# Kernel tuning notes

Measured on AMD Instinct MI355X. Metric: run time of the kernel, lower is better.

## Reference

```python
import jax, jax.numpy as jnp
import numpy as np

N_NODES = 100000
N_EDGES = 3200000
DIM = 64


def setup_inputs() -> dict:
    key = jax.random.key(0)
    k1, k2, k3, k4, k5, k6 = jax.random.split(key, 6)
    lap_rows = jax.random.randint(k1, (N_EDGES,), 0, N_NODES, dtype=jnp.int32)
    lap_cols = jax.random.randint(k2, (N_EDGES,), 0, N_NODES, dtype=jnp.int32)
    # normalized-Laplacian-like positive values
    lap_vals = jax.random.uniform(k3, (N_EDGES,), dtype=jnp.float32) * 0.1
    features = jax.random.normal(k4, (N_NODES, DIM), dtype=jnp.float32)
    scale = 1.0 / np.sqrt(DIM)
    W1 = jax.random.normal(k5, (DIM, DIM), dtype=jnp.float32) * scale
    b1 = jnp.zeros((DIM,), dtype=jnp.float32)
    W2 = jax.random.normal(k6, (DIM, DIM), dtype=jnp.float32) * scale
    b2 = jnp.zeros((DIM,), dtype=jnp.float32)
    return {
        "lap_rows": lap_rows, "lap_cols": lap_cols, "lap_vals": lap_vals,
        "features": features, "W1": W1, "b1": b1, "W2": W2, "b2": b2,
    }


def reference(lap_rows, lap_cols, lap_vals, features, W1, b1, W2, b2):
    # x = L @ features  (COO SpMM: gather source rows, scale, scatter-add to dest)
    msgs = lap_vals[:, None] * features[lap_cols]            # [E, D]
    x = jax.ops.segment_sum(msgs, lap_rows, num_segments=N_NODES)  # [N, D]
    # output = (L+I) E W1 + (L E * E) W2
    inter_part1 = (features + x) @ W1 + b1                   # [N, D_out]
    inter_part2 = (x * features) @ W2 + b2                   # [N, D_out]
    return inter_part1 + inter_part2
```

## Files before the change

kernel.cpp:

```cpp
#include <hip/hip_runtime.h>
#include <hip/hip_fp16.h>

#define DIM 64
#define RPB 64
#define RPB_SHIFT 6
#define SUP_SHIFT 11
#define SB_MAX 64
#define CAP 3072
#define CAPK (CAP / 1024)
#define HTILE_H 16384
#define HTILE1 8192
#define HTILE2 4096

typedef _Float16 half8 __attribute__((ext_vector_type(8)));
typedef float    f32x4 __attribute__((ext_vector_type(4)));
typedef float    f32x2 __attribute__((ext_vector_type(2)));

template <bool HI>
__device__ __forceinline__ __half2 q2h(unsigned int w)
{
    f32x2 f = __builtin_amdgcn_cvt_pk_f32_fp8(w, HI);
    return __floats2half2_rn(f[0], f[1]);
}

__global__ __launch_bounds__(256) void scatter_kernel(
    const int* __restrict__ rows, const int* __restrict__ cols,
    const float* __restrict__ vals, const float* __restrict__ feat,
    float* __restrict__ x, int E)
{
    unsigned long long t = (unsigned long long)blockIdx.x * blockDim.x + threadIdx.x;
    int e = (int)(t >> 6);
    int d = (int)(t & 63);
    if (e >= E) return;
    int r = rows[e];
    int c = cols[e];
    float v = vals[e];
    float f = feat[(size_t)c * DIM + d];
    atomicAdd(&x[(size_t)r * DIM + d], v * f);
}

__global__ __launch_bounds__(256) void cvt_kernel(
    const float* __restrict__ f, __half* __restrict__ h, int n2)
{
    int i = blockIdx.x * blockDim.x + threadIdx.x;
    if (i < n2) {
        float2 v = ((const float2*)f)[i];
        __half2 o;
        o.x = __float2half(v.x);
        o.y = __float2half(v.y);
        ((__half2*)h)[i] = o;
    }
}

__global__ __launch_bounds__(1024) void prep_kernel(
    const float* __restrict__ feat, __half* __restrict__ featH,
    unsigned char* __restrict__ featQ,
    const int* __restrict__ rows, int* __restrict__ gcnt,
    int n8, int NC, int E, int B)
{
    if ((int)blockIdx.x < NC) {
        int i = blockIdx.x * 1024 + threadIdx.x;
        if (i < n8) {
            const float4* src = (const float4*)(feat + (size_t)i * 8);
            float4 a = src[0], b = src[1];
            __half2 h0 = __floats2half2_rn(a.x, a.y);
            __half2 h1 = __floats2half2_rn(a.z, a.w);
            __half2 h2 = __floats2half2_rn(b.x, b.y);
            __half2 h3 = __floats2half2_rn(b.z, b.w);
            float4 ho;
            ho.x = __builtin_bit_cast(float, h0);
            ho.y = __builtin_bit_cast(float, h1);
            ho.z = __builtin_bit_cast(float, h2);
            ho.w = __builtin_bit_cast(float, h3);
            *(float4*)(featH + (size_t)i * 8) = ho;
            unsigned int q0 = __builtin_amdgcn_cvt_pk_fp8_f32(a.x, a.y, 0, false);
            q0 = __builtin_amdgcn_cvt_pk_fp8_f32(a.z, a.w, (int)q0, true);
            unsigned int q1 = __builtin_amdgcn_cvt_pk_fp8_f32(b.x, b.y, 0, false);
            q1 = __builtin_amdgcn_cvt_pk_fp8_f32(b.z, b.w, (int)q1, true);
            uint2 qo; qo.x = q0; qo.y = q1;
            *(uint2*)(featQ + (size_t)i * 8) = qo;
        }
    } else {
        extern __shared__ int lcnt[];
        for (int i = threadIdx.x; i < B; i += 1024) lcnt[i] = 0;
        __syncthreads();
        int base = ((int)blockIdx.x - NC) * HTILE_H;
#pragma unroll
        for (int k = 0; k < HTILE_H / 1024; ++k) {
            int e = base + k * 1024 + threadIdx.x;
            if (e < E) atomicAdd(&lcnt[rows[e] >> RPB_SHIFT], 1);
        }
        __syncthreads();
        for (int i = threadIdx.x; i < B; i += 1024)
            if (lcnt[i]) atomicAdd(&gcnt[i], lcnt[i]);
    }
}

__global__ __launch_bounds__(1024) void scan_kernel(
    const int* __restrict__ gcnt, int* __restrict__ offs, int* __restrict__ cursors,
    int* __restrict__ soffs, int* __restrict__ scursors, int B, int SB, int E)
{
    __shared__ int lds[2048];
    int t = threadIdx.x;
    int c0 = (t < B) ? gcnt[t] : 0;
    int c1 = (t + 1024 < B) ? gcnt[t + 1024] : 0;
    lds[t] = c0;
    lds[t + 1024] = c1;
    __syncthreads();
    for (int off = 1; off < 2048; off <<= 1) {
        int a = (t >= off) ? lds[t - off] : 0;
        int b = lds[t + 1024 - off];
        __syncthreads();
        lds[t] += a;
        lds[t + 1024] += b;
        __syncthreads();
    }
    if (t < B) {
        int e = lds[t] - c0;
        offs[t] = e; cursors[t] = e;
        if ((t & 31) == 0) { soffs[t >> 5] = e; scursors[t >> 5] = e; }
    }
    int t2 = t + 1024;
    if (t2 < B) {
        int e = lds[t2] - c1;
        offs[t2] = e; cursors[t2] = e;
        if ((t2 & 31) == 0) { soffs[t2 >> 5] = e; scursors[t2 >> 5] = e; }
    }
    if (t == 0) { offs[B] = E; soffs[SB] = E; }
}

__global__ __launch_bounds__(1024) void superbin_kernel(
    const int* __restrict__ rows, const int* __restrict__ cols,
    const float* __restrict__ vals, int* __restrict__ scursors,
    unsigned long long* __restrict__ sorted1, int E, int SB)
{
    __shared__ int cnt[SB_MAX];
    __shared__ int bse[SB_MAX];
    const int tid = threadIdx.x;
    if (tid < SB) cnt[tid] = 0;
    __syncthreads();
    const int tbase = blockIdx.x * HTILE1;
    int rr[HTILE1 / 1024];
#pragma unroll
    for (int k = 0; k < HTILE1 / 1024; ++k) {
        int e = tbase + k * 1024 + tid;
        rr[k] = (e < E) ? rows[e] : -1;
        if (rr[k] >= 0) atomicAdd(&cnt[rr[k] >> SUP_SHIFT], 1);
    }
    __syncthreads();
    if (tid < SB) {
        int c = cnt[tid];
        bse[tid] = c ? atomicAdd(&scursors[tid], c) : 0;
        cnt[tid] = 0;
    }
    __syncthreads();
#pragma unroll
    for (int k = 0; k < HTILE1 / 1024; ++k) {
        int e = tbase + k * 1024 + tid;
        if (rr[k] >= 0) {
            int r  = rr[k];
            int sb = r >> SUP_SHIFT;
            int slot = bse[sb] + atomicAdd(&cnt[sb], 1);
            unsigned long long pk =
                ((unsigned long long)__float_as_uint(vals[e]) << 32) |
                ((unsigned long long)(r & 2047) << 17) |
                (unsigned)cols[e];
            sorted1[slot] = pk;
        }
    }
}

__global__ __launch_bounds__(1024) void finebin_kernel(
    const unsigned long long* __restrict__ sorted1, const int* __restrict__ soffs,
    int* __restrict__ cursors, unsigned long long* __restrict__ sorted2,
    int E, int B, int SB)
{
    extern __shared__ int l[];
    int* cnt  = l;
    int* bse  = l + B;
    int* sofl = l + 2 * B;
    const int tid = threadIdx.x;
    if (tid <= SB) sofl[tid] = soffs[tid];
    for (int i = tid; i < B; i += 1024) cnt[i] = 0;
    __syncthreads();

    const int tbase = blockIdx.x * HTILE2;
    int sb0 = 0;
    {
        int lo = 0, hi = SB - 1;
        while (lo < hi) {
            int mid = (lo + hi + 1) >> 1;
            if (sofl[mid] <= tbase) lo = mid; else hi = mid - 1;
        }
        sb0 = lo;
    }

    unsigned long long pkr[HTILE2 / 1024];
    int fidr[HTILE2 / 1024];
#pragma unroll
    for (int k = 0; k < HTILE2 / 1024; ++k) {
        int i = tbase + k * 1024 + tid;
        if (i < E) {
            pkr[k] = sorted1[i];
            int sb = sb0;
            while (sofl[sb + 1] <= i) sb++;
            fidr[k] = (sb << 5) + (int)((pkr[k] >> 23) & 31);
            atomicAdd(&cnt[fidr[k]], 1);
        } else fidr[k] = -1;
    }
    __syncthreads();
    for (int i = tid; i < B; i += 1024) {
        int c = cnt[i];
        bse[i] = c ? atomicAdd(&cursors[i], c) : 0;
    }
    __syncthreads();
    for (int i = tid; i < B; i += 1024) cnt[i] = 0;
    __syncthreads();
#pragma unroll
    for (int k = 0; k < HTILE2 / 1024; ++k) {
        if (fidr[k] >= 0) {
            int f = fidr[k];
            int slot = bse[f] + atomicAdd(&cnt[f], 1);
            sorted2[slot] = pkr[k];
        }
    }
}

__global__ __launch_bounds__(1024, 8) void reduce_fused_mfma_kernel(
    const unsigned long long* __restrict__ sorted, const int* __restrict__ offs,
    const unsigned char* __restrict__ featQ, const __half* __restrict__ featH,
    const float* __restrict__ W1, const float* __restrict__ b1,
    const float* __restrict__ W2, const float* __restrict__ b2,
    float* __restrict__ out, int N)
{
    __shared__ unsigned long long spk[CAP];
    __shared__ int rcnt[RPB];
    __shared__ int rbase[RPB];
    __shared__ float xs[RPB][DIM + 4];
    __shared__ half8 Wl[1024];
    __shared__ float biasl[DIM];

    const int tid = threadIdx.x;
    const int b   = blockIdx.x;
    const int w    = tid >> 6;
    const int lane = tid & 63;

    {
        int t    = tid >> 8;
        int c    = (tid >> 6) & 3;
        int quad = (tid >> 4) & 3;
        int m    = tid & 15;
        const float* Wsrc = (t < 2) ? W1 : W2;
        int kbase = (t & 1) * 32 + quad * 8;
        int col   = c * 16 + m;
        half8 wv;
#pragma unroll
        for (int j = 0; j < 8; ++j)
            wv[j] = (_Float16)Wsrc[(kbase + j) * DIM + col];
        Wl[tid] = wv;
        if (tid < DIM) biasl[tid] = b1[tid] + b2[tid];
    }

    const int s    = offs[b];
    const int tend = offs[b + 1];
    int nl = tend - s;
    if (nl > CAP) nl = CAP;

    if (tid < RPB) rcnt[tid] = 0;
    __syncthreads();

    unsigned long long pkreg[CAPK];
#pragma unroll
    for (int k = 0; k < CAPK; ++k) {
        int i = k * 1024 + tid;
        pkreg[k] = (i < nl) ? sorted[s + i] : 0ull;
    }
#pragma unroll
    for (int k = 0; k < CAPK; ++k) {
        int i = k * 1024 + tid;
        if (i < nl) atomicAdd(&rcnt[(int)((pkreg[k] >> 17) & (RPB - 1))], 1);
    }
    __syncthreads();

    if (tid < 64) {
        int c = rcnt[tid];
        int v = c;
#pragma unroll
        for (int off = 1; off < 64; off <<= 1) {
            int u = __shfl_up(v, off, 64);
            if (tid >= off) v += u;
        }
        rbase[tid] = v - c;
        rcnt[tid]  = 0;
    }
    __syncthreads();

#pragma unroll
    for (int k = 0; k < CAPK; ++k) {
        int i = k * 1024 + tid;
        if (i < nl) {
            int rl  = (int)((pkreg[k] >> 17) & (RPB - 1));
            int idx = atomicAdd(&rcnt[rl], 1);
            spk[rbase[rl] + idx] = pkreg[k];
        }
    }
    __syncthreads();

    const int eg   = lane >> 3;
    const int sub  = lane & 7;
    const int rowbase = b * RPB;

#pragma unroll
    for (int j = 0; j < RPB / 16; ++j) {
        int rl = w + 16 * j;
        int rs = rbase[rl];
        int rt = rs + rcnt[rl];

        __half2 hacc[4];
#pragma unroll
        for (int q = 0; q < 4; ++q) hacc[q] = __floats2half2_rn(0.f, 0.f);

        int i = rs + eg;
        for (; i + 24 < rt; i += 32) {
            unsigned long long pk0 = spk[i];
            unsigned long long pk1 = spk[i + 8];
            unsigned long long pk2 = spk[i + 16];
            unsigned long long pk3 = spk[i + 24];
            uint2 q0 = *(const uint2*)(featQ + ((size_t)(pk0 & 0x1FFFFu) << 6) + sub * 8);
            uint2 q1 = *(const uint2*)(featQ + ((size_t)(pk1 & 0x1FFFFu) << 6) + sub * 8);
            uint2 q2 = *(const uint2*)(featQ + ((size_t)(pk2 & 0x1FFFFu) << 6) + sub * 8);
            uint2 q3 = *(const uint2*)(featQ + ((size_t)(pk3 & 0x1FFFFu) << 6) + sub * 8);
            __half2 v0 = __float2half2_rn(__uint_as_float((unsigned)(pk0 >> 32)));
            __half2 v1 = __float2half2_rn(__uint_as_float((unsigned)(pk1 >> 32)));
            __half2 v2 = __float2half2_rn(__uint_as_float((unsigned)(pk2 >> 32)));
            __half2 v3 = __float2half2_rn(__uint_as_float((unsigned)(pk3 >> 32)));
            hacc[0] = __hfma2(v0, q2h<false>(q0.x), hacc[0]);
            hacc[1] = __hfma2(v0, q2h<true >(q0.x), hacc[1]);
            hacc[2] = __hfma2(v0, q2h<false>(q0.y), hacc[2]);
            hacc[3] = __hfma2(v0, q2h<true >(q0.y), hacc[3]);
            hacc[0] = __hfma2(v1, q2h<false>(q1.x), hacc[0]);
            hacc[1] = __hfma2(v1, q2h<true >(q1.x), hacc[1]);
            hacc[2] = __hfma2(v1, q2h<false>(q1.y), hacc[2]);
            hacc[3] = __hfma2(v1, q2h<true >(q1.y), hacc[3]);
            hacc[0] = __hfma2(v2, q2h<false>(q2.x), hacc[0]);
            hacc[1] = __hfma2(v2, q2h<true >(q2.x), hacc[1]);
            hacc[2] = __hfma2(v2, q2h<false>(q2.y), hacc[2]);
            hacc[3] = __hfma2(v2, q2h<true >(q2.y), hacc[3]);
            hacc[0] = __hfma2(v3, q2h<false>(q3.x), hacc[0]);
            hacc[1] = __hfma2(v3, q2h<true >(q3.x), hacc[1]);
            hacc[2] = __hfma2(v3, q2h<false>(q3.y), hacc[2]);
            hacc[3] = __hfma2(v3, q2h<true >(q3.y), hacc[3]);
        }
        for (; i < rt; i += 8) {
            unsigned long long pk0 = spk[i];
            uint2 q0 = *(const uint2*)(featQ + ((size_t)(pk0 & 0x1FFFFu) << 6) + sub * 8);
            __half2 v0 = __float2half2_rn(__uint_as_float((unsigned)(pk0 >> 32)));
            hacc[0] = __hfma2(v0, q2h<false>(q0.x), hacc[0]);
            hacc[1] = __hfma2(v0, q2h<true >(q0.x), hacc[1]);
            hacc[2] = __hfma2(v0, q2h<false>(q0.y), hacc[2]);
            hacc[3] = __hfma2(v0, q2h<true >(q0.y), hacc[3]);
        }

        float acc[8];
#pragma unroll
        for (int q = 0; q < 4; ++q) {
            acc[2 * q]     = __low2float(hacc[q]);
            acc[2 * q + 1] = __high2float(hacc[q]);
        }
#pragma unroll
        for (int off = 8; off < 64; off <<= 1) {
#pragma unroll
            for (int q = 0; q < 8; ++q)
                acc[q] += __shfl_xor(acc[q], off, 64);
        }

        if (eg == 0) {
            float4 o; o.x = acc[0]; o.y = acc[1]; o.z = acc[2]; o.w = acc[3];
            *(float4*)&xs[rl][sub * 8] = o;
        } else if (eg == 1) {
            float4 o; o.x = acc[4]; o.y = acc[5]; o.z = acc[6]; o.w = acc[7];
            *(float4*)&xs[rl][sub * 8 + 4] = o;
        }
    }
    __syncthreads();

    if (tend - s > CAP) {
        for (int e = s + CAP + tid; e < tend; e += 1024) {
            unsigned long long pk = sorted[e];
            int rl = (int)((pk >> 17) & (RPB - 1));
            float v = __uint_as_float((unsigned)(pk >> 32));
            int c = (int)(pk & 0x1FFFFu);
            for (int d = 0; d < DIM; ++d)
                atomicAdd(&xs[rl][d], v * __half2float(featH[(size_t)c * DIM + d]));
        }
        __syncthreads();
    }

    {
        const int m    = lane & 15;
        const int quad = lane >> 4;
        const int tile = w >> 2;
        const int cw   = w & 3;

        const int fb = cw * 64 + quad * 16 + m;
        half8 wf0 = Wl[fb];
        half8 wf1 = Wl[fb + 256];
        half8 wf2 = Wl[fb + 512];
        half8 wf3 = Wl[fb + 768];
        float bias = biasl[cw * 16 + m];

        int rowl = tile * 16 + m;
        int grow = rowbase + rowl;
        int rldr = (grow < N) ? grow : (N - 1);
        const __half* fp = featH + (size_t)rldr * DIM + quad * 8;
        half8 flo = *(const half8*)(fp);
        half8 fhi = *(const half8*)(fp + 32);
        const float* xp = &xs[rowl][quad * 8];
        float4 xl0 = *(const float4*)(xp);
        float4 xl1 = *(const float4*)(xp + 4);
        float4 xh0 = *(const float4*)(xp + 32);
        float4 xh1 = *(const float4*)(xp + 36);

        half8 alo, ahi, blo, bhi;
        _Float16 xv;
        xv = (_Float16)xl0.x; alo[0] = flo[0] + xv; blo[0] = flo[0] * xv;
        xv = (_Float16)xl0.y; alo[1] = flo[1] + xv; blo[1] = flo[1] * xv;
        xv = (_Float16)xl0.z; alo[2] = flo[2] + xv; blo[2] = flo[2] * xv;
        xv = (_Float16)xl0.w; alo[3] = flo[3] + xv; blo[3] = flo[3] * xv;
        xv = (_Float16)xl1.x; alo[4] = flo[4] + xv; blo[4] = flo[4] * xv;
        xv = (_Float16)xl1.y; alo[5] = flo[5] + xv; blo[5] = flo[5] * xv;
        xv = (_Float16)xl1.z; alo[6] = flo[6] + xv; blo[6] = flo[6] * xv;
        xv = (_Float16)xl1.w; alo[7] = flo[7] + xv; blo[7] = flo[7] * xv;
        xv = (_Float16)xh0.x; ahi[0] = fhi[0] + xv; bhi[0] = fhi[0] * xv;
        xv = (_Float16)xh0.y; ahi[1] = fhi[1] + xv; bhi[1] = fhi[1] * xv;
        xv = (_Float16)xh0.z; ahi[2] = fhi[2] + xv; bhi[2] = fhi[2] * xv;
        xv = (_Float16)xh0.w; ahi[3] = fhi[3] + xv; bhi[3] = fhi[3] * xv;
        xv = (_Float16)xh1.x; ahi[4] = fhi[4] + xv; bhi[4] = fhi[4] * xv;
        xv = (_Float16)xh1.y; ahi[5] = fhi[5] + xv; bhi[5] = fhi[5] * xv;
        xv = (_Float16)xh1.z; ahi[6] = fhi[6] + xv; bhi[6] = fhi[6] * xv;
        xv = (_Float16)xh1.w; ahi[7] = fhi[7] + xv; bhi[7] = fhi[7] * xv;

        f32x4 a0 = { bias, bias, bias, bias };
        a0 = __builtin_amdgcn_mfma_f32_16x16x32_f16(alo, wf0, a0, 0, 0, 0);
        a0 = __builtin_amdgcn_mfma_f32_16x16x32_f16(ahi, wf1, a0, 0, 0, 0);
        a0 = __builtin_amdgcn_mfma_f32_16x16x32_f16(blo, wf2, a0, 0, 0, 0);
        a0 = __builtin_amdgcn_mfma_f32_16x16x32_f16(bhi, wf3, a0, 0, 0, 0);

#pragma unroll
        for (int reg = 0; reg < 4; ++reg) {
            int orow = rowbase + tile * 16 + quad * 4 + reg;
            if (orow < N)
                out[(size_t)orow * DIM + cw * 16 + m] = a0[reg];
        }
    }
}

__global__ __launch_bounds__(256) void transform_mfma_kernel(
    const __half* __restrict__ featH, const float* __restrict__ x,
    const float* __restrict__ W1, const float* __restrict__ b1,
    const float* __restrict__ W2, const float* __restrict__ b2,
    float* __restrict__ out, int N)
{
    const int lane = threadIdx.x & 63;
    const int m    = lane & 15;
    const int quad = lane >> 4;

    half8 wfrag[4][4];
#pragma unroll
    for (int t = 0; t < 4; ++t) {
        const float* Wsrc = (t < 2) ? W1 : W2;
        int kbase = (t & 1) * 32 + quad * 8;
#pragma unroll
        for (int c = 0; c < 4; ++c) {
            int col = c * 16 + m;
            half8 w;
#pragma unroll
            for (int j = 0; j < 8; ++j)
                w[j] = (_Float16)Wsrc[(kbase + j) * DIM + col];
            wfrag[t][c] = w;
        }
    }
    float bias[4];
#pragma unroll
    for (int c = 0; c < 4; ++c)
        bias[c] = b1[c * 16 + m] + b2[c * 16 + m];

    const int ntiles = (N + 15) / 16;
    const int wid    = (int)((blockIdx.x * blockDim.x + threadIdx.x) >> 6);
    const int nwaves = (int)((gridDim.x * blockDim.x) >> 6);

    for (int tile = wid; tile < ntiles; tile += nwaves) {
        int row  = tile * 16 + m;
        int rldr = (row < N) ? row : (N - 1);
        const __half* fp = featH + (size_t)rldr * DIM + quad * 8;
        const float*  xp = x     + (size_t)rldr * DIM + quad * 8;
        half8 flo = *(const half8*)(fp);
        half8 fhi = *(const half8*)(fp + 32);
        float4 xl0 = *(const float4*)(xp);
        float4 xl1 = *(const float4*)(xp + 4);
        float4 xh0 = *(const float4*)(xp + 32);
        float4 xh1 = *(const float4*)(xp + 36);

        half8 alo, ahi, blo, bhi;
        _Float16 xv;
        xv = (_Float16)xl0.x; alo[0] = flo[0] + xv; blo[0] = flo[0] * xv;
        xv = (_Float16)xl0.y; alo[1] = flo[1] + xv; blo[1] = flo[1] * xv;
        xv = (_Float16)xl0.z; alo[2] = flo[2] + xv; blo[2] = flo[2] * xv;
        xv = (_Float16)xl0.w; alo[3] = flo[3] + xv; blo[3] = flo[3] * xv;
        xv = (_Float16)xl1.x; alo[4] = flo[4] + xv; blo[4] = flo[4] * xv;
        xv = (_Float16)xl1.y; alo[5] = flo[5] + xv; blo[5] = flo[5] * xv;
        xv = (_Float16)xl1.z; alo[6] = flo[6] + xv; blo[6] = flo[6] * xv;
        xv = (_Float16)xl1.w; alo[7] = flo[7] + xv; blo[7] = flo[7] * xv;
        xv = (_Float16)xh0.x; ahi[0] = fhi[0] + xv; bhi[0] = fhi[0] * xv;
        xv = (_Float16)xh0.y; ahi[1] = fhi[1] + xv; bhi[1] = fhi[1] * xv;
        xv = (_Float16)xh0.z; ahi[2] = fhi[2] + xv; bhi[2] = fhi[2] * xv;
        xv = (_Float16)xh0.w; ahi[3] = fhi[3] + xv; bhi[3] = fhi[3] * xv;
        xv = (_Float16)xh1.x; ahi[4] = fhi[4] + xv; bhi[4] = fhi[4] * xv;
        xv = (_Float16)xh1.y; ahi[5] = fhi[5] + xv; bhi[5] = fhi[5] * xv;
        xv = (_Float16)xh1.z; ahi[6] = fhi[6] + xv; bhi[6] = fhi[6] * xv;
        xv = (_Float16)xh1.w; ahi[7] = fhi[7] + xv; bhi[7] = fhi[7] * xv;

        f32x4 acc[4];
#pragma unroll
        for (int c = 0; c < 4; ++c) {
            f32x4 a0 = { bias[c], bias[c], bias[c], bias[c] };
            a0 = __builtin_amdgcn_mfma_f32_16x16x32_f16(alo, wfrag[0][c], a0, 0, 0, 0);
            a0 = __builtin_amdgcn_mfma_f32_16x16x32_f16(ahi, wfrag[1][c], a0, 0, 0, 0);
            a0 = __builtin_amdgcn_mfma_f32_16x16x32_f16(blo, wfrag[2][c], a0, 0, 0, 0);
            a0 = __builtin_amdgcn_mfma_f32_16x16x32_f16(bhi, wfrag[3][c], a0, 0, 0, 0);
            acc[c] = a0;
        }

#pragma unroll
        for (int reg = 0; reg < 4; ++reg) {
            int orow = tile * 16 + quad * 4 + reg;
            if (orow < N) {
#pragma unroll
                for (int c = 0; c < 4; ++c)
                    out[(size_t)orow * DIM + c * 16 + m] = acc[c][reg];
            }
        }
    }
}

extern "C" void kernel_launch(void* const* d_in, const int* in_sizes, int n_in,
                              void* d_out, int out_size, void* d_ws, size_t ws_size,
                              hipStream_t stream)
{
    const int*   rows = (const int*)d_in[0];
    const int*   cols = (const int*)d_in[1];
    const float* vals = (const float*)d_in[2];
    const float* feat = (const float*)d_in[3];
    const float* W1   = (const float*)d_in[4];
    const float* b1   = (const float*)d_in[5];
    const float* W2   = (const float*)d_in[6];
    const float* b2   = (const float*)d_in[7];
    float* out = (float*)d_out;

    const int E  = in_sizes[0];
    const int N  = in_sizes[3] / DIM;
    const int B  = (N + RPB - 1) / RPB;
    const int SB = (B + 31) / 32;

    char* ws = (char*)d_ws;
    size_t xBytes     = (size_t)N * DIM * sizeof(float);
    size_t hBytes     = (((size_t)N * DIM * sizeof(__half)) + 255) / 256 * 256;
    size_t qBytes     = (((size_t)N * DIM) + 255) / 256 * 256;
    size_t offsBytes  = (((size_t)(B + 1) * sizeof(int)) + 255) / 256 * 256;
    size_t cursBytes  = (((size_t)B * sizeof(int)) + 255) / 256 * 256;
    size_t soffBytes  = (((size_t)(SB + 1) * sizeof(int)) + 255) / 256 * 256;
    size_t scurBytes  = (((size_t)SB * sizeof(int)) + 255) / 256 * 256;
    size_t sortBytes  = (size_t)E * 8;

    float*              x        = (float*)ws;
    __half*             featH    = (__half*)(ws + xBytes);
    unsigned char*      featQ    = (unsigned char*)(ws + xBytes + hBytes);
    int*                offs     = (int*)(ws + xBytes + hBytes + qBytes);
    int*                cursors  = (int*)(ws + xBytes + hBytes + qBytes + offsBytes);
    int*                soffs    = (int*)(ws + xBytes + hBytes + qBytes + offsBytes + cursBytes);
    int*                scursors = (int*)(ws + xBytes + hBytes + qBytes + offsBytes + cursBytes + soffBytes);
    unsigned long long* sorted1  = (unsigned long long*)(ws + xBytes + hBytes + qBytes + offsBytes +
                                                         cursBytes + soffBytes + scurBytes);
    unsigned long long* sorted2  = sorted1 + E;
    size_t need = xBytes + hBytes + qBytes + offsBytes + cursBytes + soffBytes + scurBytes + 2 * sortBytes;

    if (ws_size >= need && B <= 2048 && SB <= SB_MAX && N <= 131072) {
        const int n8  = N * DIM / 8;
        const int NC  = (n8 + 1023) / 1024;
        const int NTH = (E + HTILE_H - 1) / HTILE_H;
        const int NT1 = (E + HTILE1 - 1) / HTILE1;
        const int NT2 = (E + HTILE2 - 1) / HTILE2;
        hipMemsetAsync(offs, 0, (size_t)(B + 1) * sizeof(int), stream);
        prep_kernel<<<NC + NTH, 1024, (size_t)B * 4, stream>>>(
            feat, featH, featQ, rows, offs, n8, NC, E, B);
        scan_kernel<<<1, 1024, 0, stream>>>(offs, offs, cursors, soffs, scursors, B, SB, E);
        superbin_kernel<<<NT1, 1024, 0, stream>>>(rows, cols, vals, scursors, sorted1, E, SB);
        finebin_kernel<<<NT2, 1024, (size_t)(2 * B + SB + 1) * 4, stream>>>(
            sorted1, soffs, cursors, sorted2, E, B, SB);
        reduce_fused_mfma_kernel<<<B, 1024, 0, stream>>>(sorted2, offs, featQ, featH,
                                                         W1, b1, W2, b2, out, N);
    } else {
        cvt_kernel<<<(N * DIM / 2 + 255) / 256, 256, 0, stream>>>(feat, featH, N * DIM / 2);
        hipMemsetAsync(x, 0, xBytes, stream);
        unsigned long long threads = (unsigned long long)E * DIM;
        unsigned int blocks = (unsigned int)((threads + 255ull) / 256ull);
        scatter_kernel<<<blocks, 256, 0, stream>>>(rows, cols, vals, feat, x, E);
        transform_mfma_kernel<<<640, 256, 0, stream>>>(featH, x, W1, b1, W2, b2, out, N);
    }
}
```

Baseline: 241.7 us.

## Replace per-row LDS regrouping with fixed-point LDS atomic accumulation

```diff
diff --git a/kernel.cpp b/kernel.cpp
--- a/kernel.cpp
+++ b/kernel.cpp
@@ -2,25 +2,24 @@
 #include <hip/hip_fp16.h>
 
 #define DIM 64
-#define RPB 64
-#define RPB_SHIFT 6
+#define RPB 128
+#define RPB_SHIFT 7
 #define SUP_SHIFT 11
 #define SB_MAX 64
-#define CAP 3072
-#define CAPK (CAP / 1024)
 #define HTILE_H 16384
-#define HTILE1 8192
+#define HTILE1 4096
 #define HTILE2 4096
+#define XSCALE 4194304.0f
+#define XINV   2.384185791015625e-7f
 
 typedef _Float16 half8 __attribute__((ext_vector_type(8)));
 typedef float    f32x4 __attribute__((ext_vector_type(4)));
 typedef float    f32x2 __attribute__((ext_vector_type(2)));
 
 template <bool HI>
-__device__ __forceinline__ __half2 q2h(unsigned int w)
-{
-    f32x2 f = __builtin_amdgcn_cvt_pk_f32_fp8(w, HI);
-    return __floats2half2_rn(f[0], f[1]);
+__device__ __forceinline__ f32x2 q2f(unsigned int w)
+{
+    return __builtin_amdgcn_cvt_pk_f32_fp8(w, HI);
 }
 
 __global__ __launch_bounds__(256) void scatter_kernel(
@@ -118,13 +117,13 @@
     if (t < B) {
         int e = lds[t] - c0;
         offs[t] = e; cursors[t] = e;
-        if ((t & 31) == 0) { soffs[t >> 5] = e; scursors[t >> 5] = e; }
+        if ((t & 15) == 0) { soffs[t >> 4] = e; scursors[t >> 4] = e; }
     }
     int t2 = t + 1024;
     if (t2 < B) {
         int e = lds[t2] - c1;
         offs[t2] = e; cursors[t2] = e;
-        if ((t2 & 31) == 0) { soffs[t2 >> 5] = e; scursors[t2 >> 5] = e; }
+        if ((t2 & 15) == 0) { soffs[t2 >> 4] = e; scursors[t2 >> 4] = e; }
     }
     if (t == 0) { offs[B] = E; soffs[SB] = E; }
 }
@@ -204,7 +203,7 @@
             pkr[k] = sorted1[i];
             int sb = sb0;
             while (sofl[sb + 1] <= i) sb++;
-            fidr[k] = (sb << 5) + (int)((pkr[k] >> 23) & 31);
+            fidr[k] = (sb << 4) + (int)((pkr[k] >> 24) & 15);
             atomicAdd(&cnt[fidr[k]], 1);
         } else fidr[k] = -1;
     }
@@ -226,24 +225,19 @@
     }
 }
 
-__global__ __launch_bounds__(1024, 8) void reduce_fused_mfma_kernel(
+__global__ __launch_bounds__(1024, 4) void reduce_fused_mfma_kernel(
     const unsigned long long* __restrict__ sorted, const int* __restrict__ offs,
     const unsigned char* __restrict__ featQ, const __half* __restrict__ featH,
     const float* __restrict__ W1, const float* __restrict__ b1,
     const float* __restrict__ W2, const float* __restrict__ b2,
     float* __restrict__ out, int N)
 {
-    __shared__ unsigned long long spk[CAP];
-    __shared__ int rcnt[RPB];
-    __shared__ int rbase[RPB];
-    __shared__ float xs[RPB][DIM + 4];
+    __shared__ int   xi[RPB][DIM + 4];
     __shared__ half8 Wl[1024];
     __shared__ float biasl[DIM];
 
     const int tid = threadIdx.x;
     const int b   = blockIdx.x;
-    const int w    = tid >> 6;
-    const int lane = tid & 63;
 
     {
         int t    = tid >> 8;
@@ -260,147 +254,66 @@
         Wl[tid] = wv;
         if (tid < DIM) biasl[tid] = b1[tid] + b2[tid];
     }
-
-    const int s    = offs[b];
-    const int tend = offs[b + 1];
-    int nl = tend - s;
-    if (nl > CAP) nl = CAP;
-
-    if (tid < RPB) rcnt[tid] = 0;
-    __syncthreads();
-
-    unsigned long long pkreg[CAPK];
-#pragma unroll
-    for (int k = 0; k < CAPK; ++k) {
-        int i = k * 1024 + tid;
-        pkreg[k] = (i < nl) ? sorted[s + i] : 0ull;
-    }
-#pragma unroll
-    for (int k = 0; k < CAPK; ++k) {
-        int i = k * 1024 + tid;
-        if (i < nl) atomicAdd(&rcnt[(int)((pkreg[k] >> 17) & (RPB - 1))], 1);
-    }
-    __syncthreads();
-
-    if (tid < 64) {
-        int c = rcnt[tid];
-        int v = c;
-#pragma unroll
-        for (int off = 1; off < 64; off <<= 1) {
-            int u = __shfl_up(v, off, 64);
-            if (tid >= off) v += u;
-        }
-        rbase[tid] = v - c;
-        rcnt[tid]  = 0;
-    }
-    __syncthreads();
-
-#pragma unroll
-    for (int k = 0; k < CAPK; ++k) {
-        int i = k * 1024 + tid;
-        if (i < nl) {
-            int rl  = (int)((pkreg[k] >> 17) & (RPB - 1));
-            int idx = atomicAdd(&rcnt[rl], 1);
-            spk[rbase[rl] + idx] = pkreg[k];
-        }
-    }
-    __syncthreads();
-
-    const int eg   = lane >> 3;
-    const int sub  = lane & 7;
+    for (int i = tid; i < RPB * (DIM + 4); i += 1024) ((int*)xi)[i] = 0;
+    __syncthreads();
+
+    const int s = offs[b], t = offs[b + 1];
+    const int grp = tid >> 3;
+    const int sub = tid & 7;
     const int rowbase = b * RPB;
 
-#pragma unroll
-    for (int j = 0; j < RPB / 16; ++j) {
-        int rl = w + 16 * j;
-        int rs = rbase[rl];
-        int rt = rs + rcnt[rl];
-
-        __half2 hacc[4];
-#pragma unroll
-        for (int q = 0; q < 4; ++q) hacc[q] = __floats2half2_rn(0.f, 0.f);
-
-        int i = rs + eg;
-        for (; i + 24 < rt; i += 32) {
-            unsigned long long pk0 = spk[i];
-            unsigned long long pk1 = spk[i + 8];
-            unsigned long long pk2 = spk[i + 16];
-            unsigned long long pk3 = spk[i + 24];
-            uint2 q0 = *(const uint2*)(featQ + ((size_t)(pk0 & 0x1FFFFu) << 6) + sub * 8);
-            uint2 q1 = *(const uint2*)(featQ + ((size_t)(pk1 & 0x1FFFFu) << 6) + sub * 8);
-            uint2 q2 = *(const uint2*)(featQ + ((size_t)(pk2 & 0x1FFFFu) << 6) + sub * 8);
-            uint2 q3 = *(const uint2*)(featQ + ((size_t)(pk3 & 0x1FFFFu) << 6) + sub * 8);
-            __half2 v0 = __float2half2_rn(__uint_as_float((unsigned)(pk0 >> 32)));
-            __half2 v1 = __float2half2_rn(__uint_as_float((unsigned)(pk1 >> 32)));
-            __half2 v2 = __float2half2_rn(__uint_as_float((unsigned)(pk2 >> 32)));
-            __half2 v3 = __float2half2_rn(__uint_as_float((unsigned)(pk3 >> 32)));
-            hacc[0] = __hfma2(v0, q2h<false>(q0.x), hacc[0]);
-            hacc[1] = __hfma2(v0, q2h<true >(q0.x), hacc[1]);
-            hacc[2] = __hfma2(v0, q2h<false>(q0.y), hacc[2]);
-            hacc[3] = __hfma2(v0, q2h<true >(q0.y), hacc[3]);
-            hacc[0] = __hfma2(v1, q2h<false>(q1.x), hacc[0]);
-            hacc[1] = __hfma2(v1, q2h<true >(q1.x), hacc[1]);
-            hacc[2] = __hfma2(v1, q2h<false>(q1.y), hacc[2]);
-            hacc[3] = __hfma2(v1, q2h<true >(q1.y), hacc[3]);
-            hacc[0] = __hfma2(v2, q2h<false>(q2.x), hacc[0]);
-            hacc[1] = __hfma2(v2, q2h<true >(q2.x), hacc[1]);
-            hacc[2] = __hfma2(v2, q2h<false>(q2.y), hacc[2]);
-            hacc[3] = __hfma2(v2, q2h<true >(q2.y), hacc[3]);
-            hacc[0] = __hfma2(v3, q2h<false>(q3.x), hacc[0]);
-            hacc[1] = __hfma2(v3, q2h<true >(q3.x), hacc[1]);
-            hacc[2] = __hfma2(v3, q2h<false>(q3.y), hacc[2]);
-            hacc[3] = __hfma2(v3, q2h<true >(q3.y), hacc[3]);
-        }
-        for (; i < rt; i += 8) {
-            unsigned long long pk0 = spk[i];
-            uint2 q0 = *(const uint2*)(featQ + ((size_t)(pk0 & 0x1FFFFu) << 6) + sub * 8);
-            __half2 v0 = __float2half2_rn(__uint_as_float((unsigned)(pk0 >> 32)));
-            hacc[0] = __hfma2(v0, q2h<false>(q0.x), hacc[0]);
-            hacc[1] = __hfma2(v0, q2h<true >(q0.x), hacc[1]);
-            hacc[2] = __hfma2(v0, q2h<false>(q0.y), hacc[2]);
-            hacc[3] = __hfma2(v0, q2h<true >(q0.y), hacc[3]);
-        }
-
-        float acc[8];
-#pragma unroll
-        for (int q = 0; q < 4; ++q) {
-            acc[2 * q]     = __low2float(hacc[q]);
-            acc[2 * q + 1] = __high2float(hacc[q]);
-        }
-#pragma unroll
-        for (int off = 8; off < 64; off <<= 1) {
-#pragma unroll
-            for (int q = 0; q < 8; ++q)
-                acc[q] += __shfl_xor(acc[q], off, 64);
-        }
-
-        if (eg == 0) {
-            float4 o; o.x = acc[0]; o.y = acc[1]; o.z = acc[2]; o.w = acc[3];
-            *(float4*)&xs[rl][sub * 8] = o;
-        } else if (eg == 1) {
-            float4 o; o.x = acc[4]; o.y = acc[5]; o.z = acc[6]; o.w = acc[7];
-            *(float4*)&xs[rl][sub * 8 + 4] = o;
-        }
-    }
-    __syncthreads();
-
-    if (tend - s > CAP) {
-        for (int e = s + CAP + tid; e < tend; e += 1024) {
-            unsigned long long pk = sorted[e];
-            int rl = (int)((pk >> 17) & (RPB - 1));
-            float v = __uint_as_float((unsigned)(pk >> 32));
-            int c = (int)(pk & 0x1FFFFu);
-            for (int d = 0; d < DIM; ++d)
-                atomicAdd(&xs[rl][d], v * __half2float(featH[(size_t)c * DIM + d]));
-        }
-        __syncthreads();
-    }
-
-    {
-        const int m    = lane & 15;
-        const int quad = lane >> 4;
-        const int tile = w >> 2;
-        const int cw   = w & 3;
+#define EDGE_ACC(PK, Q)                                                      \
+    {                                                                        \
+        int   rl = (int)(((PK) >> 17) & (RPB - 1));                          \
+        float v  = __uint_as_float((unsigned)((PK) >> 32)) * XSCALE;         \
+        int* base = &xi[rl][sub * 8];                                        \
+        f32x2 f0 = q2f<false>((Q).x);                                        \
+        f32x2 f1 = q2f<true >((Q).x);                                        \
+        f32x2 f2 = q2f<false>((Q).y);                                        \
+        f32x2 f3 = q2f<true >((Q).y);                                        \
+        atomicAdd(base + 0, (int)(f0[0] * v));                               \
+        atomicAdd(base + 1, (int)(f0[1] * v));                               \
+        atomicAdd(base + 2, (int)(f1[0] * v));                               \
+        atomicAdd(base + 3, (int)(f1[1] * v));                               \
+        atomicAdd(base + 4, (int)(f2[0] * v));                               \
+        atomicAdd(base + 5, (int)(f2[1] * v));                               \
+        atomicAdd(base + 6, (int)(f3[0] * v));                               \
+        atomicAdd(base + 7, (int)(f3[1] * v));                               \
+    }
+
+    int i = s + grp;
+    for (; i + 384 < t; i += 512) {
+        unsigned long long pk0 = sorted[i];
+        unsigned long long pk1 = sorted[i + 128];
+        unsigned long long pk2 = sorted[i + 256];
+        unsigned long long pk3 = sorted[i + 384];
+        uint2 q0 = *(const uint2*)(featQ + ((size_t)(pk0 & 0x1FFFFu) << 6) + sub * 8);
+        uint2 q1 = *(const uint2*)(featQ + ((size_t)(pk1 & 0x1FFFFu) << 6) + sub * 8);
+        uint2 q2 = *(const uint2*)(featQ + ((size_t)(pk2 & 0x1FFFFu) << 6) + sub * 8);
+        uint2 q3 = *(const uint2*)(featQ + ((size_t)(pk3 & 0x1FFFFu) << 6) + sub * 8);
+        EDGE_ACC(pk0, q0)
+        EDGE_ACC(pk1, q1)
+        EDGE_ACC(pk2, q2)
+        EDGE_ACC(pk3, q3)
+    }
+    for (; i < t; i += 128) {
+        unsigned long long pk0 = sorted[i];
+        uint2 q0 = *(const uint2*)(featQ + ((size_t)(pk0 & 0x1FFFFu) << 6) + sub * 8);
+        EDGE_ACC(pk0, q0)
+    }
+#undef EDGE_ACC
+    __syncthreads();
+
+    const int w    = tid >> 6;
+    const int lane = tid & 63;
+    const int m    = lane & 15;
+    const int quad = lane >> 4;
+
+#pragma unroll
+    for (int it = 0; it < 2; ++it) {
+        int task = w + 16 * it;
+        int tile = task >> 2;
+        int cw   = task & 3;
 
         const int fb = cw * 64 + quad * 16 + m;
         half8 wf0 = Wl[fb];
@@ -415,7 +328,87 @@
         const __half* fp = featH + (size_t)rldr * DIM + quad * 8;
         half8 flo = *(const half8*)(fp);
         half8 fhi = *(const half8*)(fp + 32);
-        const float* xp = &xs[rowl][quad * 8];
+        const int* xp = &xi[rowl][quad * 8];
+        int4 xl0 = *(const int4*)(xp);
+        int4 xl1 = *(const int4*)(xp + 4);
+        int4 xh0 = *(const int4*)(xp + 32);
+        int4 xh1 = *(const int4*)(xp + 36);
+
+        half8 alo, ahi, blo, bhi;
+        _Float16 xv;
+        xv = (_Float16)((float)xl0.x * XINV); alo[0] = flo[0] + xv; blo[0] = flo[0] * xv;
+        xv = (_Float16)((float)xl0.y * XINV); alo[1] = flo[1] + xv; blo[1] = flo[1] * xv;
+        xv = (_Float16)((float)xl0.z * XINV); alo[2] = flo[2] + xv; blo[2] = flo[2] * xv;
+        xv = (_Float16)((float)xl0.w * XINV); alo[3] = flo[3] + xv; blo[3] = flo[3] * xv;
+        xv = (_Float16)((float)xl1.x * XINV); alo[4] = flo[4] + xv; blo[4] = flo[4] * xv;
+        xv = (_Float16)((float)xl1.y * XINV); alo[5] = flo[5] + xv; blo[5] = flo[5] * xv;
+        xv = (_Float16)((float)xl1.z * XINV); alo[6] = flo[6] + xv; blo[6] = flo[6] * xv;
+        xv = (_Float16)((float)xl1.w * XINV); alo[7] = flo[7] + xv; blo[7] = flo[7] * xv;
+        xv = (_Float16)((float)xh0.x * XINV); ahi[0] = fhi[0] + xv; bhi[0] = fhi[0] * xv;
+        xv = (_Float16)((float)xh0.y * XINV); ahi[1] = fhi[1] + xv; bhi[1] = fhi[1] * xv;
+        xv = (_Float16)((float)xh0.z * XINV); ahi[2] = fhi[2] + xv; bhi[2] = fhi[2] * xv;
+        xv = (_Float16)((float)xh0.w * XINV); ahi[3] = fhi[3] + xv; bhi[3] = fhi[3] * xv;
+        xv = (_Float16)((float)xh1.x * XINV); ahi[4] = fhi[4] + xv; bhi[4] = fhi[4] * xv;
+        xv = (_Float16)((float)xh1.y * XINV); ahi[5] = fhi[5] + xv; bhi[5] = fhi[5] * xv;
+        xv = (_Float16)((float)xh1.z * XINV); ahi[6] = fhi[6] + xv; bhi[6] = fhi[6] * xv;
+        xv = (_Float16)((float)xh1.w * XINV); ahi[7] = fhi[7] + xv; bhi[7] = fhi[7] * xv;
+
+        f32x4 a0 = { bias, bias, bias, bias };
+        a0 = __builtin_amdgcn_mfma_f32_16x16x32_f16(alo, wf0, a0, 0, 0, 0);
+        a0 = __builtin_amdgcn_mfma_f32_16x16x32_f16(ahi, wf1, a0, 0, 0, 0);
+        a0 = __builtin_amdgcn_mfma_f32_16x16x32_f16(blo, wf2, a0, 0, 0, 0);
+        a0 = __builtin_amdgcn_mfma_f32_16x16x32_f16(bhi, wf3, a0, 0, 0, 0);
+
+#pragma unroll
+        for (int reg = 0; reg < 4; ++reg) {
+            int orow = rowbase + tile * 16 + quad * 4 + reg;
+            if (orow < N)
+                out[(size_t)orow * DIM + cw * 16 + m] = a0[reg];
+        }
+    }
+}
+
+__global__ __launch_bounds__(256) void transform_mfma_kernel(
+    const __half* __restrict__ featH, const float* __restrict__ x,
+    const float* __restrict__ W1, const float* __restrict__ b1,
+    const float* __restrict__ W2, const float* __restrict__ b2,
+    float* __restrict__ out, int N)
+{
+    const int lane = threadIdx.x & 63;
+    const int m    = lane & 15;
+    const int quad = lane >> 4;
+
+    half8 wfrag[4][4];
+#pragma unroll
+    for (int t = 0; t < 4; ++t) {
+        const float* Wsrc = (t < 2) ? W1 : W2;
+        int kbase = (t & 1) * 32 + quad * 8;
+#pragma unroll
+        for (int c = 0; c < 4; ++c) {
+            int col = c * 16 + m;
+            half8 w;
+#pragma unroll
+            for (int j = 0; j < 8; ++j)
+                w[j] = (_Float16)Wsrc[(kbase + j) * DIM + col];
+            wfrag[t][c] = w;
+        }
+    }
+    float bias[4];
+#pragma unroll
+    for (int c = 0; c < 4; ++c)
+        bias[c] = b1[c * 16 + m] + b2[c * 16 + m];
+
+    const int ntiles = (N + 15) / 16;
+    const int wid    = (int)((blockIdx.x * blockDim.x + threadIdx.x) >> 6);
+    const int nwaves = (int)((gridDim.x * blockDim.x) >> 6);
+
+    for (int tile = wid; tile < ntiles; tile += nwaves) {
+        int row  = tile * 16 + m;
+        int rldr = (row < N) ? row : (N - 1);
+        const __half* fp = featH + (size_t)rldr * DIM + quad * 8;
+        const float*  xp = x     + (size_t)rldr * DIM + quad * 8;
+        half8 flo = *(const half8*)(fp);
+        half8 fhi = *(const half8*)(fp + 32);
         float4 xl0 = *(const float4*)(xp);
         float4 xl1 = *(const float4*)(xp + 4);
         float4 xh0 = *(const float4*)(xp + 32);
@@ -440,86 +433,6 @@
         xv = (_Float16)xh1.z; ahi[6] = fhi[6] + xv; bhi[6] = fhi[6] * xv;
         xv = (_Float16)xh1.w; ahi[7] = fhi[7] + xv; bhi[7] = fhi[7] * xv;
 
-        f32x4 a0 = { bias, bias, bias, bias };
-        a0 = __builtin_amdgcn_mfma_f32_16x16x32_f16(alo, wf0, a0, 0, 0, 0);
-        a0 = __builtin_amdgcn_mfma_f32_16x16x32_f16(ahi, wf1, a0, 0, 0, 0);
-        a0 = __builtin_amdgcn_mfma_f32_16x16x32_f16(blo, wf2, a0, 0, 0, 0);
-        a0 = __builtin_amdgcn_mfma_f32_16x16x32_f16(bhi, wf3, a0, 0, 0, 0);
-
-#pragma unroll
-        for (int reg = 0; reg < 4; ++reg) {
-            int orow = rowbase + tile * 16 + quad * 4 + reg;
-            if (orow < N)
-                out[(size_t)orow * DIM + cw * 16 + m] = a0[reg];
-        }
-    }
-}
-
-__global__ __launch_bounds__(256) void transform_mfma_kernel(
-    const __half* __restrict__ featH, const float* __restrict__ x,
-    const float* __restrict__ W1, const float* __restrict__ b1,
-    const float* __restrict__ W2, const float* __restrict__ b2,
-    float* __restrict__ out, int N)
-{
-    const int lane = threadIdx.x & 63;
-    const int m    = lane & 15;
-    const int quad = lane >> 4;
-
-    half8 wfrag[4][4];
-#pragma unroll
-    for (int t = 0; t < 4; ++t) {
-        const float* Wsrc = (t < 2) ? W1 : W2;
-        int kbase = (t & 1) * 32 + quad * 8;
-#pragma unroll
-        for (int c = 0; c < 4; ++c) {
-            int col = c * 16 + m;
-            half8 w;
-#pragma unroll
-            for (int j = 0; j < 8; ++j)
-                w[j] = (_Float16)Wsrc[(kbase + j) * DIM + col];
-            wfrag[t][c] = w;
-        }
-    }
-    float bias[4];
-#pragma unroll
-    for (int c = 0; c < 4; ++c)
-        bias[c] = b1[c * 16 + m] + b2[c * 16 + m];
-
-    const int ntiles = (N + 15) / 16;
-    const int wid    = (int)((blockIdx.x * blockDim.x + threadIdx.x) >> 6);
-    const int nwaves = (int)((gridDim.x * blockDim.x) >> 6);
-
-    for (int tile = wid; tile < ntiles; tile += nwaves) {
-        int row  = tile * 16 + m;
-        int rldr = (row < N) ? row : (N - 1);
-        const __half* fp = featH + (size_t)rldr * DIM + quad * 8;
-        const float*  xp = x     + (size_t)rldr * DIM + quad * 8;
-        half8 flo = *(const half8*)(fp);
-        half8 fhi = *(const half8*)(fp + 32);
-        float4 xl0 = *(const float4*)(xp);
-        float4 xl1 = *(const float4*)(xp + 4);
-        float4 xh0 = *(const float4*)(xp + 32);
-        float4 xh1 = *(const float4*)(xp + 36);
-
-        half8 alo, ahi, blo, bhi;
-        _Float16 xv;
-        xv = (_Float16)xl0.x; alo[0] = flo[0] + xv; blo[0] = flo[0] * xv;
-        xv = (_Float16)xl0.y; alo[1] = flo[1] + xv; blo[1] = flo[1] * xv;
-        xv = (_Float16)xl0.z; alo[2] = flo[2] + xv; blo[2] = flo[2] * xv;
-        xv = (_Float16)xl0.w; alo[3] = flo[3] + xv; blo[3] = flo[3] * xv;
-        xv = (_Float16)xl1.x; alo[4] = flo[4] + xv; blo[4] = flo[4] * xv;
-        xv = (_Float16)xl1.y; alo[5] = flo[5] + xv; blo[5] = flo[5] * xv;
-        xv = (_Float16)xl1.z; alo[6] = flo[6] + xv; blo[6] = flo[6] * xv;
-        xv = (_Float16)xl1.w; alo[7] = flo[7] + xv; blo[7] = flo[7] * xv;
-        xv = (_Float16)xh0.x; ahi[0] = fhi[0] + xv; bhi[0] = fhi[0] * xv;
-        xv = (_Float16)xh0.y; ahi[1] = fhi[1] + xv; bhi[1] = fhi[1] * xv;
-        xv = (_Float16)xh0.z; ahi[2] = fhi[2] + xv; bhi[2] = fhi[2] * xv;
-        xv = (_Float16)xh0.w; ahi[3] = fhi[3] + xv; bhi[3] = fhi[3] * xv;
-        xv = (_Float16)xh1.x; ahi[4] = fhi[4] + xv; bhi[4] = fhi[4] * xv;
-        xv = (_Float16)xh1.y; ahi[5] = fhi[5] + xv; bhi[5] = fhi[5] * xv;
-        xv = (_Float16)xh1.z; ahi[6] = fhi[6] + xv; bhi[6] = fhi[6] * xv;
-        xv = (_Float16)xh1.w; ahi[7] = fhi[7] + xv; bhi[7] = fhi[7] * xv;
-
         f32x4 acc[4];
 #pragma unroll
         for (int c = 0; c < 4; ++c) {
@@ -560,7 +473,7 @@
     const int E  = in_sizes[0];
     const int N  = in_sizes[3] / DIM;
     const int B  = (N + RPB - 1) / RPB;
-    const int SB = (B + 31) / 32;
+    const int SB = (B + 15) / 16;
 
     char* ws = (char*)d_ws;
     size_t xBytes     = (size_t)N * DIM * sizeof(float);
```

After: 268.2 us. 11.0% more time.

## Split sorted edge records into 32-bit index and fp16 value arrays

Applied to the files above, without the earlier changes.

```diff
diff --git a/kernel.cpp b/kernel.cpp
--- a/kernel.cpp
+++ b/kernel.cpp
@@ -6,10 +6,10 @@
 #define RPB_SHIFT 6
 #define SUP_SHIFT 11
 #define SB_MAX 64
-#define CAP 3072
+#define CAP 4096
 #define CAPK (CAP / 1024)
 #define HTILE_H 16384
-#define HTILE1 8192
+#define HTILE1 4096
 #define HTILE2 4096
 
 typedef _Float16 half8 __attribute__((ext_vector_type(8)));
@@ -132,7 +132,8 @@
 __global__ __launch_bounds__(1024) void superbin_kernel(
     const int* __restrict__ rows, const int* __restrict__ cols,
     const float* __restrict__ vals, int* __restrict__ scursors,
-    unsigned long long* __restrict__ sorted1, int E, int SB)
+    unsigned int* __restrict__ sa1, unsigned short* __restrict__ sv1,
+    int E, int SB)
 {
     __shared__ int cnt[SB_MAX];
     __shared__ int bse[SB_MAX];
@@ -161,18 +162,16 @@
             int r  = rr[k];
             int sb = r >> SUP_SHIFT;
             int slot = bse[sb] + atomicAdd(&cnt[sb], 1);
-            unsigned long long pk =
-                ((unsigned long long)__float_as_uint(vals[e]) << 32) |
-                ((unsigned long long)(r & 2047) << 17) |
-                (unsigned)cols[e];
-            sorted1[slot] = pk;
+            sa1[slot] = ((unsigned)(r & 2047) << 17) | (unsigned)cols[e];
+            sv1[slot] = __builtin_bit_cast(unsigned short, __float2half(vals[e]));
         }
     }
 }
 
 __global__ __launch_bounds__(1024) void finebin_kernel(
-    const unsigned long long* __restrict__ sorted1, const int* __restrict__ soffs,
-    int* __restrict__ cursors, unsigned long long* __restrict__ sorted2,
+    const unsigned int* __restrict__ sa1, const unsigned short* __restrict__ sv1,
+    const int* __restrict__ soffs, int* __restrict__ cursors,
+    unsigned int* __restrict__ sa2, unsigned short* __restrict__ sv2,
     int E, int B, int SB)
 {
     extern __shared__ int l[];
@@ -195,16 +194,18 @@
         sb0 = lo;
     }
 
-    unsigned long long pkr[HTILE2 / 1024];
+    unsigned int   ar[HTILE2 / 1024];
+    unsigned short vr[HTILE2 / 1024];
     int fidr[HTILE2 / 1024];
 #pragma unroll
     for (int k = 0; k < HTILE2 / 1024; ++k) {
         int i = tbase + k * 1024 + tid;
         if (i < E) {
-            pkr[k] = sorted1[i];
+            ar[k] = sa1[i];
+            vr[k] = sv1[i];
             int sb = sb0;
             while (sofl[sb + 1] <= i) sb++;
-            fidr[k] = (sb << 5) + (int)((pkr[k] >> 23) & 31);
+            fidr[k] = (sb << 5) + (int)((ar[k] >> 23) & 31);
             atomicAdd(&cnt[fidr[k]], 1);
         } else fidr[k] = -1;
     }
@@ -221,19 +222,22 @@
         if (fidr[k] >= 0) {
             int f = fidr[k];
             int slot = bse[f] + atomicAdd(&cnt[f], 1);
-            sorted2[slot] = pkr[k];
+            sa2[slot] = ar[k];
+            sv2[slot] = vr[k];
         }
     }
 }
 
 __global__ __launch_bounds__(1024, 8) void reduce_fused_mfma_kernel(
-    const unsigned long long* __restrict__ sorted, const int* __restrict__ offs,
+    const unsigned int* __restrict__ sa, const unsigned short* __restrict__ sv,
+    const int* __restrict__ offs,
     const unsigned char* __restrict__ featQ, const __half* __restrict__ featH,
     const float* __restrict__ W1, const float* __restrict__ b1,
     const float* __restrict__ W2, const float* __restrict__ b2,
     float* __restrict__ out, int N)
 {
-    __shared__ unsigned long long spk[CAP];
+    __shared__ unsigned int   spkA[CAP];
+    __shared__ unsigned short spkV[CAP];
     __shared__ int rcnt[RPB];
     __shared__ int rbase[RPB];
     __shared__ float xs[RPB][DIM + 4];
@@ -269,16 +273,18 @@
     if (tid < RPB) rcnt[tid] = 0;
     __syncthreads();
 
-    unsigned long long pkreg[CAPK];
+    unsigned int   areg[CAPK];
+    unsigned short vreg[CAPK];
 #pragma unroll
     for (int k = 0; k < CAPK; ++k) {
         int i = k * 1024 + tid;
-        pkreg[k] = (i < nl) ? sorted[s + i] : 0ull;
+        areg[k] = (i < nl) ? __builtin_nontemporal_load(sa + s + i) : 0u;
+        vreg[k] = (i < nl) ? __builtin_nontemporal_load(sv + s + i) : (unsigned short)0;
     }
 #pragma unroll
     for (int k = 0; k < CAPK; ++k) {
         int i = k * 1024 + tid;
-        if (i < nl) atomicAdd(&rcnt[(int)((pkreg[k] >> 17) & (RPB - 1))], 1);
+        if (i < nl) atomicAdd(&rcnt[(int)((areg[k] >> 17) & (RPB - 1))], 1);
     }
     __syncthreads();
 
@@ -299,9 +305,11 @@
     for (int k = 0; k < CAPK; ++k) {
         int i = k * 1024 + tid;
         if (i < nl) {
-            int rl  = (int)((pkreg[k] >> 17) & (RPB - 1));
+            int rl  = (int)((areg[k] >> 17) & (RPB - 1));
             int idx = atomicAdd(&rcnt[rl], 1);
-            spk[rbase[rl] + idx] = pkreg[k];
+            int slot = rbase[rl] + idx;
+            spkA[slot] = areg[k];
+            spkV[slot] = vreg[k];
         }
     }
     __syncthreads();
@@ -309,6 +317,9 @@
     const int eg   = lane >> 3;
     const int sub  = lane & 7;
     const int rowbase = b * RPB;
+
+#define GATHER(A) (*(const uint2*)(featQ + ((size_t)((A) & 0x1FFFFu) << 6) + sub * 8))
+#define VB(V) __half2half2(__builtin_bit_cast(__half, (V)))
 
 #pragma unroll
     for (int j = 0; j < RPB / 16; ++j) {
@@ -322,18 +333,18 @@
 
         int i = rs + eg;
         for (; i + 24 < rt; i += 32) {
-            unsigned long long pk0 = spk[i];
-            unsigned long long pk1 = spk[i + 8];
-            unsigned long long pk2 = spk[i + 16];
-            unsigned long long pk3 = spk[i + 24];
-            uint2 q0 = *(const uint2*)(featQ + ((size_t)(pk0 & 0x1FFFFu) << 6) + sub * 8);
-            uint2 q1 = *(const uint2*)(featQ + ((size_t)(pk1 & 0x1FFFFu) << 6) + sub * 8);
-            uint2 q2 = *(const uint2*)(featQ + ((size_t)(pk2 & 0x1FFFFu) << 6) + sub * 8);
-            uint2 q3 = *(const uint2*)(featQ + ((size_t)(pk3 & 0x1FFFFu) << 6) + sub * 8);
-            __half2 v0 = __float2half2_rn(__uint_as_float((unsigned)(pk0 >> 32)));
-            __half2 v1 = __float2half2_rn(__uint_as_float((unsigned)(pk1 >> 32)));
-            __half2 v2 = __float2half2_rn(__uint_as_float((unsigned)(pk2 >> 32)));
-            __half2 v3 = __float2half2_rn(__uint_as_float((unsigned)(pk3 >> 32)));
+            unsigned int a0 = spkA[i];
+            unsigned int a1 = spkA[i + 8];
+            unsigned int a2 = spkA[i + 16];
+            unsigned int a3 = spkA[i + 24];
+            uint2 q0 = GATHER(a0);
+            uint2 q1 = GATHER(a1);
+            uint2 q2 = GATHER(a2);
+            uint2 q3 = GATHER(a3);
+            __half2 v0 = VB(spkV[i]);
+            __half2 v1 = VB(spkV[i + 8]);
+            __half2 v2 = VB(spkV[i + 16]);
+            __half2 v3 = VB(spkV[i + 24]);
             hacc[0] = __hfma2(v0, q2h<false>(q0.x), hacc[0]);
             hacc[1] = __hfma2(v0, q2h<true >(q0.x), hacc[1]);
             hacc[2] = __hfma2(v0, q2h<false>(q0.y), hacc[2]);
@@ -352,9 +363,9 @@
             hacc[3] = __hfma2(v3, q2h<true >(q3.y), hacc[3]);
         }
         for (; i < rt; i += 8) {
-            unsigned long long pk0 = spk[i];
-            uint2 q0 = *(const uint2*)(featQ + ((size_t)(pk0 & 0x1FFFFu) << 6) + sub * 8);
-            __half2 v0 = __float2half2_rn(__uint_as_float((unsigned)(pk0 >> 32)));
+            unsigned int a0 = spkA[i];
+            uint2 q0 = GATHER(a0);
+            __half2 v0 = VB(spkV[i]);
             hacc[0] = __hfma2(v0, q2h<false>(q0.x), hacc[0]);
             hacc[1] = __hfma2(v0, q2h<true >(q0.x), hacc[1]);
             hacc[2] = __hfma2(v0, q2h<false>(q0.y), hacc[2]);
@@ -382,14 +393,16 @@
             *(float4*)&xs[rl][sub * 8 + 4] = o;
         }
     }
+#undef GATHER
+#undef VB
     __syncthreads();
 
     if (tend - s > CAP) {
         for (int e = s + CAP + tid; e < tend; e += 1024) {
-            unsigned long long pk = sorted[e];
-            int rl = (int)((pk >> 17) & (RPB - 1));
-            float v = __uint_as_float((unsigned)(pk >> 32));
-            int c = (int)(pk & 0x1FFFFu);
+            unsigned int a = sa[e];
+            float v = __half2float(__builtin_bit_cast(__half, sv[e]));
+            int rl = (int)((a >> 17) & (RPB - 1));
+            int c  = (int)(a & 0x1FFFFu);
             for (int d = 0; d < DIM; ++d)
                 atomicAdd(&xs[rl][d], v * __half2float(featH[(size_t)c * DIM + d]));
         }
@@ -570,19 +583,23 @@
     size_t cursBytes  = (((size_t)B * sizeof(int)) + 255) / 256 * 256;
     size_t soffBytes  = (((size_t)(SB + 1) * sizeof(int)) + 255) / 256 * 256;
     size_t scurBytes  = (((size_t)SB * sizeof(int)) + 255) / 256 * 256;
-    size_t sortBytes  = (size_t)E * 8;
-
-    float*              x        = (float*)ws;
-    __half*             featH    = (__half*)(ws + xBytes);
-    unsigned char*      featQ    = (unsigned char*)(ws + xBytes + hBytes);
-    int*                offs     = (int*)(ws + xBytes + hBytes + qBytes);
-    int*                cursors  = (int*)(ws + xBytes + hBytes + qBytes + offsBytes);
-    int*                soffs    = (int*)(ws + xBytes + hBytes + qBytes + offsBytes + cursBytes);
-    int*                scursors = (int*)(ws + xBytes + hBytes + qBytes + offsBytes + cursBytes + soffBytes);
-    unsigned long long* sorted1  = (unsigned long long*)(ws + xBytes + hBytes + qBytes + offsBytes +
-                                                         cursBytes + soffBytes + scurBytes);
-    unsigned long long* sorted2  = sorted1 + E;
-    size_t need = xBytes + hBytes + qBytes + offsBytes + cursBytes + soffBytes + scurBytes + 2 * sortBytes;
+    size_t saBytes    = (((size_t)E * 4) + 255) / 256 * 256;
+    size_t svBytes    = (((size_t)E * 2) + 255) / 256 * 256;
+
+    float*          x        = (float*)ws;
+    __half*         featH    = (__half*)(ws + xBytes);
+    unsigned char*  featQ    = (unsigned char*)(ws + xBytes + hBytes);
+    int*            offs     = (int*)(ws + xBytes + hBytes + qBytes);
+    int*            cursors  = (int*)(ws + xBytes + hBytes + qBytes + offsBytes);
+    int*            soffs    = (int*)(ws + xBytes + hBytes + qBytes + offsBytes + cursBytes);
+    int*            scursors = (int*)(ws + xBytes + hBytes + qBytes + offsBytes + cursBytes + soffBytes);
+    char*           pb       = ws + xBytes + hBytes + qBytes + offsBytes + cursBytes + soffBytes + scurBytes;
+    unsigned int*   sa1      = (unsigned int*)(pb);
+    unsigned short* sv1      = (unsigned short*)(pb + saBytes);
+    unsigned int*   sa2      = (unsigned int*)(pb + saBytes + svBytes);
+    unsigned short* sv2      = (unsigned short*)(pb + 2 * saBytes + svBytes);
+    size_t need = xBytes + hBytes + qBytes + offsBytes + cursBytes + soffBytes + scurBytes
+                + 2 * (saBytes + svBytes);
 
     if (ws_size >= need && B <= 2048 && SB <= SB_MAX && N <= 131072) {
         const int n8  = N * DIM / 8;
@@ -594,10 +611,10 @@
         prep_kernel<<<NC + NTH, 1024, (size_t)B * 4, stream>>>(
             feat, featH, featQ, rows, offs, n8, NC, E, B);
         scan_kernel<<<1, 1024, 0, stream>>>(offs, offs, cursors, soffs, scursors, B, SB, E);
-        superbin_kernel<<<NT1, 1024, 0, stream>>>(rows, cols, vals, scursors, sorted1, E, SB);
+        superbin_kernel<<<NT1, 1024, 0, stream>>>(rows, cols, vals, scursors, sa1, sv1, E, SB);
         finebin_kernel<<<NT2, 1024, (size_t)(2 * B + SB + 1) * 4, stream>>>(
-            sorted1, soffs, cursors, sorted2, E, B, SB);
-        reduce_fused_mfma_kernel<<<B, 1024, 0, stream>>>(sorted2, offs, featQ, featH,
+            sa1, sv1, soffs, cursors, sa2, sv2, E, B, SB);
+        reduce_fused_mfma_kernel<<<B, 1024, 0, stream>>>(sa2, sv2, offs, featQ, featH,
                                                          W1, b1, W2, b2, out, N);
     } else {
         cvt_kernel<<<(N * DIM / 2 + 255) / 256, 256, 0, stream>>>(feat, featH, N * DIM / 2);
```

New measurement: 257.3 us. +6.5%, slower.
